# Kernel optimization log

Measured on AMD Instinct MI355X. Metric: run time of the kernel, lower is better.

The kernel has to match this reference:

```python
import jax, jax.numpy as jnp
import numpy as np

N_NODES = 100000
N_EDGES = 1600000
IN_CH, CH1, CH2 = 256, 256, 128


def gcn_conv(x, W, b, src, dst, ew, n):
    """PyG GCNConv: h = x @ W; out[i] = sum_j norm_ij * h[j] + b, with self-loops
    (weight 1.0) and symmetric normalization D^-1/2 A D^-1/2."""
    loop = jnp.arange(n)
    src_f = jnp.concatenate([src, loop])
    dst_f = jnp.concatenate([dst, loop])
    ew_f = jnp.concatenate([ew, jnp.ones((n,), dtype=x.dtype)])
    deg = jax.ops.segment_sum(ew_f, dst_f, num_segments=n)  # weighted in-degree incl self-loop
    dinv = jnp.where(deg > 0, jax.lax.rsqrt(deg), 0.0)
    norm = dinv[src_f] * ew_f * dinv[dst_f]                  # [E+N]
    h = x @ W                                                # [N, C_out]
    msg = h[src_f] * norm[:, None]                           # gather + scale, [E+N, C_out]
    out = jax.ops.segment_sum(msg, dst_f, num_segments=n)   # scatter-add to targets
    return out + b


def setup_inputs() -> dict:
    key = jax.random.key(0)
    ks = jax.random.split(key, 7)
    x = jax.random.normal(ks[0], (N_NODES, IN_CH), dtype=jnp.float32)
    edge_index = jax.random.randint(ks[1], (2, N_EDGES), 0, N_NODES, dtype=jnp.int64)
    edge_weight = jax.random.uniform(ks[2], (N_EDGES,), dtype=jnp.float32)
    # Glorot-style init for GCN weights, zero bias (PyG defaults)
    W1 = jax.random.normal(ks[3], (IN_CH, CH1), dtype=jnp.float32) * (1.0 / np.sqrt(IN_CH))
    b1 = jnp.zeros((CH1,), dtype=jnp.float32)
    W2 = jax.random.normal(ks[4], (CH1, CH2), dtype=jnp.float32) * (1.0 / np.sqrt(CH1))
    b2 = jnp.zeros((CH2,), dtype=jnp.float32)
    return {"x": x, "edge_index": edge_index, "edge_weight": edge_weight,
            "W1": W1, "b1": b1, "W2": W2, "b2": b2}


def reference(x, edge_index, edge_weight, W1, b1, W2, b2):
    src, dst = edge_index[0], edge_index[1]
    n = x.shape[0]
    x1 = gcn_conv(x, W1, b1, src, dst, edge_weight, n)
    x1 = jax.nn.gelu(x1, approximate=False)  # torch F.gelu default is exact erf
    # dropout is identity in eval mode (deterministic reference)
    x2 = gcn_conv(x1, W2, b2, src, dst, edge_weight, n)
    return x2
```

## Files before the change

### kernel.cpp

```cpp
#include <hip/hip_runtime.h>
#include <math.h>


#define CH1 256
#define CH2 128
#define MAXDEG 64

using bf16x8 = __attribute__((ext_vector_type(8))) short;
using f32x4  = __attribute__((ext_vector_type(4))) float;

__device__ __forceinline__ ushort f2bf(float f) {
    unsigned u = __float_as_uint(f);
    u = u + 0x7fffu + ((u >> 16) & 1u);
    return (ushort)(u >> 16);
}
__device__ __forceinline__ float bf_lo(unsigned u) {
    return __uint_as_float(u << 16);
}
__device__ __forceinline__ float bf_hi(unsigned u) {
    return __uint_as_float(u & 0xffff0000u);
}
__device__ __forceinline__ float dinv_from(unsigned long long a) {
    return rsqrtf(1.0f + (float)(a & 0xFFFFFFFFFFull) * (1.0f / 16777216.0f));
}

__global__ void zero_acc(unsigned long long* acc, int n) {
    int i = blockIdx.x * blockDim.x + threadIdx.x;
    if (i < n) acc[i] = 0ull;
}

__global__ __launch_bounds__(256) void fused_count_cvt_w(
    const int* __restrict__ ei, const float* __restrict__ ew,
    unsigned long long* __restrict__ acc, int* __restrict__ rank,
    int E, int EB,
    const float* __restrict__ x, ushort* __restrict__ xb, int n8, int CB,
    const float* __restrict__ W1, ushort* __restrict__ W1T, int w1n, int W1B,
    const float* __restrict__ W2, ushort* __restrict__ W2T, int w2n) {
    int bid = blockIdx.x;
    if (bid < EB) {
        int base = bid * 256 + threadIdx.x;
        int stride = EB * 256;
        int e[8]; int d[8]; float w[8];
#pragma unroll
        for (int k = 0; k < 8; ++k) e[k] = base + k * stride;
#pragma unroll
        for (int k = 0; k < 8; ++k)
            if (e[k] < E) { d[k] = ei[E + e[k]]; w[k] = ew[e[k]]; }
        unsigned long long old[8];
#pragma unroll
        for (int k = 0; k < 8; ++k)
            if (e[k] < E) {
                unsigned fx = (unsigned)__float2uint_rn(w[k] * 16777216.0f);
                old[k] = atomicAdd(&acc[d[k]],
                                   (1ull << 40) | (unsigned long long)fx);
            }
#pragma unroll
        for (int k = 0; k < 8; ++k)
            if (e[k] < E) rank[e[k]] = (int)(old[k] >> 40);
    } else if (bid < EB + CB) {
        int i = (bid - EB) * 256 + threadIdx.x;
        if (i < n8) {
            float4 a = reinterpret_cast<const float4*>(x)[i * 2];
            float4 b = reinterpret_cast<const float4*>(x)[i * 2 + 1];
            uint4 o;
            o.x = (unsigned)f2bf(a.x) | ((unsigned)f2bf(a.y) << 16);
            o.y = (unsigned)f2bf(a.z) | ((unsigned)f2bf(a.w) << 16);
            o.z = (unsigned)f2bf(b.x) | ((unsigned)f2bf(b.y) << 16);
            o.w = (unsigned)f2bf(b.z) | ((unsigned)f2bf(b.w) << 16);
            reinterpret_cast<uint4*>(xb)[i] = o;
        }
    } else if (bid < EB + CB + W1B) {
        int idx = (bid - EB - CB) * 256 + threadIdx.x;
        if (idx < w1n) {
            int k = idx / CH1, nn = idx % CH1;
            W1T[nn * CH1 + k] = f2bf(W1[idx]);
        }
    } else {
        int idx = (bid - EB - CB - W1B) * 256 + threadIdx.x;
        if (idx < w2n) {
            int k = idx / CH2, nn = idx % CH2;
            W2T[nn * CH1 + k] = f2bf(W2[idx]);
        }
    }
}

__device__ __forceinline__ void gemm_body(const ushort* __restrict__ A,
                                          const ushort* __restrict__ BT,
                                          ushort* __restrict__ C,
                                          int M, int N, int K, int bx, int by) {
    __shared__ __align__(16) ushort Als[128 * 32];
    __shared__ __align__(16) ushort Bls[128 * 32];

    const int t = threadIdx.x;
    const int w = t >> 6;
    const int lane = t & 63;
    const int wr = w >> 1, wc = w & 1;
    const int row0 = bx * 128;
    const int col0 = by * 128;

    f32x4 acc[4][4] = {};

    for (int k0 = 0; k0 < K; k0 += 32) {
#pragma unroll
        for (int i = 0; i < 2; ++i) {
            int c = (w * 2 + i) * 64 + lane;
            int row = c >> 2;
            int kg = c & 3;
            int arow = row0 + row; if (arow > M - 1) arow = M - 1;
            const ushort* gA = A + (size_t)arow * K + k0 + kg * 8;
            const ushort* gB = BT + (size_t)(col0 + row) * K + k0 + kg * 8;
            __builtin_amdgcn_global_load_lds(
                (const __attribute__((address_space(1))) unsigned*)gA,
                (__attribute__((address_space(3))) unsigned*)&Als[(size_t)(w * 2 + i) * 512],
                16, 0, 0);
            __builtin_amdgcn_global_load_lds(
                (const __attribute__((address_space(1))) unsigned*)gB,
                (__attribute__((address_space(3))) unsigned*)&Bls[(size_t)(w * 2 + i) * 512],
                16, 0, 0);
        }
        __syncthreads();

        bf16x8 afr[4], bfr[4];
#pragma unroll
        for (int m = 0; m < 4; ++m)
            afr[m] = *reinterpret_cast<const bf16x8*>(
                &Als[(wr * 64 + m * 16 + (lane & 15)) * 32 + (lane >> 4) * 8]);
#pragma unroll
        for (int nn = 0; nn < 4; ++nn)
            bfr[nn] = *reinterpret_cast<const bf16x8*>(
                &Bls[(wc * 64 + nn * 16 + (lane & 15)) * 32 + (lane >> 4) * 8]);
#pragma unroll
        for (int m = 0; m < 4; ++m)
#pragma unroll
            for (int nn = 0; nn < 4; ++nn)
                acc[m][nn] = __builtin_amdgcn_mfma_f32_16x16x32_bf16(
                    afr[m], bfr[nn], acc[m][nn], 0, 0, 0);
        __syncthreads();
    }

#pragma unroll
    for (int m = 0; m < 4; ++m) {
#pragma unroll
        for (int nn = 0; nn < 4; ++nn) {
            f32x4 v = acc[m][nn];
            int col = col0 + wc * 64 + nn * 16 + (lane & 15);
#pragma unroll
            for (int j = 0; j < 4; ++j) {
                int row = row0 + wr * 64 + m * 16 + (lane >> 4) * 4 + j;
                if (row < M) C[(size_t)row * N + col] = f2bf(v[j]);
            }
        }
    }
}

__global__ __launch_bounds__(256) void gemm_bf16(const ushort* __restrict__ A,
                                                 const ushort* __restrict__ BT,
                                                 ushort* __restrict__ C,
                                                 int M, int N, int K) {
    gemm_body(A, BT, C, M, N, K, blockIdx.x, blockIdx.y);
}

__global__ __launch_bounds__(256) void scatter_gemm1(
    const int* __restrict__ ei, const float* __restrict__ ew,
    const unsigned long long* __restrict__ acc,
    const int* __restrict__ rank,
    int2* __restrict__ pairs, int E, int SB,
    const ushort* __restrict__ xb, const ushort* __restrict__ W1T,
    ushort* __restrict__ h, int M, int gx) {
    int bid = blockIdx.x;
    if (bid < SB) {
        int e = bid * 256 + threadIdx.x;
        if (e < E) {
            int s = ei[e];
            int d = ei[E + e];
            int r = min(rank[e], MAXDEG - 1);
            float dv = dinv_from(acc[s]);
            int2 p;
            p.x = s;
            p.y = __float_as_int(ew[e] * dv);
            pairs[(size_t)d * MAXDEG + r] = p;
        }
    } else {
        int g = bid - SB;
        gemm_body(xb, W1T, h, M, CH1, CH1, g % gx, g / gx);
    }
}

__device__ __forceinline__ float gelu_exact(float x) {
    return 0.5f * x * (1.0f + erff(x * 0.70710678118654752f));
}

template <int C, int APPLY_GELU, int OUT_BF16>
__global__ __launch_bounds__(256) void aggregate4(
    const ushort* __restrict__ h, const unsigned long long* __restrict__ acc64,
    const int2* __restrict__ pairs, const float* __restrict__ bias,
    void* __restrict__ outv, int n) {
    constexpr int LPE = C / 8;
    constexpr int EPG = 64 / LPE;
    int wid = threadIdx.x >> 6;
    int lane = threadIdx.x & 63;
    int g = lane / LPE;
    int l = lane % LPE;
    int node = blockIdx.x * 4 + wid;
    if (node >= n) return;

    unsigned long long a = acc64[node];
    int deg = min((int)(a >> 40), MAXDEG);
    float di = dinv_from(a);

    const int2* pb = pairs + (size_t)node * MAXDEG;
    const ushort* hl = h + l * 8;

    float acc[8];
#pragma unroll
    for (int c = 0; c < 8; ++c) acc[c] = 0.f;

    for (int t = 0; t < deg; t += 4 * EPG) {
        int2 pk[4];
        float cf[4];
        uint4 gv[4];
#pragma unroll
        for (int k = 0; k < 4; ++k) {
            int idx = t + k * EPG + g;
            int cl = min(idx, deg - 1);
            pk[k] = pb[cl];
            cf[k] = (idx < deg) ? __int_as_float(pk[k].y) : 0.f;
        }
#pragma unroll
        for (int k = 0; k < 4; ++k)
            gv[k] = *reinterpret_cast<const uint4*>(hl + (size_t)pk[k].x * C);
#pragma unroll
        for (int k = 0; k < 4; ++k) {
            acc[0] += cf[k] * bf_lo(gv[k].x);
            acc[1] += cf[k] * bf_hi(gv[k].x);
            acc[2] += cf[k] * bf_lo(gv[k].y);
            acc[3] += cf[k] * bf_hi(gv[k].y);
            acc[4] += cf[k] * bf_lo(gv[k].z);
            acc[5] += cf[k] * bf_hi(gv[k].z);
            acc[6] += cf[k] * bf_lo(gv[k].w);
            acc[7] += cf[k] * bf_hi(gv[k].w);
        }
    }

#pragma unroll
    for (int off = LPE; off < 64; off <<= 1) {
#pragma unroll
        for (int c = 0; c < 8; ++c) acc[c] += __shfl_xor(acc[c], off);
    }

    float d2 = di * di;
    uint4 sv = *reinterpret_cast<const uint4*>(hl + (size_t)node * C);
    float self[8] = {bf_lo(sv.x), bf_hi(sv.x), bf_lo(sv.y), bf_hi(sv.y),
                     bf_lo(sv.z), bf_hi(sv.z), bf_lo(sv.w), bf_hi(sv.w)};
    float4 bv0 = *reinterpret_cast<const float4*>(bias + l * 8);
    float4 bv1 = *reinterpret_cast<const float4*>(bias + l * 8 + 4);
    float bb[8] = {bv0.x, bv0.y, bv0.z, bv0.w, bv1.x, bv1.y, bv1.z, bv1.w};

    float res[8];
#pragma unroll
    for (int c = 0; c < 8; ++c) {
        float v = di * acc[c] + d2 * self[c] + bb[c];
        res[c] = APPLY_GELU ? gelu_exact(v) : v;
    }

    if (g == 0) {
        if constexpr (OUT_BF16) {
            uint4 o;
            o.x = (unsigned)f2bf(res[0]) | ((unsigned)f2bf(res[1]) << 16);
            o.y = (unsigned)f2bf(res[2]) | ((unsigned)f2bf(res[3]) << 16);
            o.z = (unsigned)f2bf(res[4]) | ((unsigned)f2bf(res[5]) << 16);
            o.w = (unsigned)f2bf(res[6]) | ((unsigned)f2bf(res[7]) << 16);
            *reinterpret_cast<uint4*>((ushort*)outv + (size_t)node * C + l * 8) = o;
        } else {
            float* op = (float*)outv + (size_t)node * C + l * 8;
            float4 o0 = {res[0], res[1], res[2], res[3]};
            float4 o1 = {res[4], res[5], res[6], res[7]};
            *reinterpret_cast<float4*>(op) = o0;
            *reinterpret_cast<float4*>(op + 4) = o1;
        }
    }
}

extern "C" void kernel_launch(void* const* d_in, const int* in_sizes, int n_in,
                              void* d_out, int out_size, void* d_ws, size_t ws_size,
                              hipStream_t stream) {
    const float* x  = (const float*)d_in[0];
    const int*   ei = (const int*)d_in[1];
    const float* ew = (const float*)d_in[2];
    const float* W1 = (const float*)d_in[3];
    const float* b1 = (const float*)d_in[4];
    const float* W2 = (const float*)d_in[5];
    const float* b2 = (const float*)d_in[6];
    float* out = (float*)d_out;

    int n = in_sizes[0] / CH1;
    int E = in_sizes[1] / 2;

    char* ws = (char*)d_ws;
    size_t off = 0;
    auto alloc = [&](size_t bytes) -> void* {
        void* p = ws + off;
        off += (bytes + 255) & ~(size_t)255;
        return p;
    };
    unsigned long long* acc64 = (unsigned long long*)alloc((size_t)n * 8);
    int*    rank     = (int*)alloc((size_t)E * 4);
    int2*   pairs    = (int2*)alloc((size_t)n * MAXDEG * 8);
    ushort* xb       = (ushort*)alloc((size_t)n * CH1 * 2);
    ushort* h        = (ushort*)alloc((size_t)n * CH1 * 2);
    ushort* x1b      = (ushort*)alloc((size_t)n * CH1 * 2);
    ushort* W1T      = (ushort*)alloc((size_t)CH1 * CH1 * 2);
    ushort* W2T      = (ushort*)alloc((size_t)CH2 * CH1 * 2);

    int gn = (n + 255) / 256;

    int EB = (E + 2047) / 2048;
    int n8 = n * CH1 / 8;
    int CB = (n8 + 255) / 256;
    int w1n = CH1 * CH1, W1B = (w1n + 255) / 256;
    int w2n = CH1 * CH2, W2B = (w2n + 255) / 256;
    zero_acc<<<gn, 256, 0, stream>>>(acc64, n);
    fused_count_cvt_w<<<EB + CB + W1B + W2B, 256, 0, stream>>>(
        ei, ew, acc64, rank, E, EB, x, xb, n8, CB,
        W1, W1T, w1n, W1B, W2, W2T, w2n);

    int SB = (E + 255) / 256;
    int gx = (n + 127) / 128;
    int G1B = gx * (CH1 / 128);
    scatter_gemm1<<<SB + G1B, 256, 0, stream>>>(ei, ew, acc64, rank,
                                                pairs, E, SB,
                                                xb, W1T, h, n, gx);

    int ngb = (n + 3) / 4;

    aggregate4<CH1, 1, 1><<<ngb, 256, 0, stream>>>(h, acc64, pairs, b1, x1b, n);

    dim3 g2(gx, CH2 / 128);
    gemm_bf16<<<g2, 256, 0, stream>>>(x1b, W2T, h, n, CH2, CH1);
    aggregate4<CH2, 0, 0><<<ngb, 256, 0, stream>>>(h, acc64, pairs, b2, out, n);
}
```

Baseline: 382.3 us.

## Fold source-side normalization into GEMM epilogue and write pairs during counting

Moves the dinv[src] factor out of the per-edge weights: GEMM1 scales each output row by its own dinv, and layer-1 aggregation multiplies its result by dinv again so GEMM2's output is already source-scaled. Because the edge weight no longer needs the source degree, pairs are written directly in the atomic counting kernel, which removes the rank array and the separate scatter pass, leaving GEMM1 as its own launch. The aggregate self term is rewritten as di*(acc+self). Edges beyond MAXDEG are now dropped instead of clamped into the last slot, and the pairs writes now sit on the atomic critical path.

```diff
diff --git a/kernel.cpp b/kernel.cpp
--- a/kernel.cpp
+++ b/kernel.cpp
@@ -31,7 +31,7 @@
 
 __global__ __launch_bounds__(256) void fused_count_cvt_w(
     const int* __restrict__ ei, const float* __restrict__ ew,
-    unsigned long long* __restrict__ acc, int* __restrict__ rank,
+    unsigned long long* __restrict__ acc, int2* __restrict__ pairs,
     int E, int EB,
     const float* __restrict__ x, ushort* __restrict__ xb, int n8, int CB,
     const float* __restrict__ W1, ushort* __restrict__ W1T, int w1n, int W1B,
@@ -40,12 +40,16 @@
     if (bid < EB) {
         int base = bid * 256 + threadIdx.x;
         int stride = EB * 256;
-        int e[8]; int d[8]; float w[8];
+        int e[8]; int s[8]; int d[8]; float w[8];
 #pragma unroll
         for (int k = 0; k < 8; ++k) e[k] = base + k * stride;
 #pragma unroll
         for (int k = 0; k < 8; ++k)
-            if (e[k] < E) { d[k] = ei[E + e[k]]; w[k] = ew[e[k]]; }
+            if (e[k] < E) {
+                s[k] = ei[e[k]];
+                d[k] = ei[E + e[k]];
+                w[k] = ew[e[k]];
+            }
         unsigned long long old[8];
 #pragma unroll
         for (int k = 0; k < 8; ++k)
@@ -56,7 +60,15 @@
             }
 #pragma unroll
         for (int k = 0; k < 8; ++k)
-            if (e[k] < E) rank[e[k]] = (int)(old[k] >> 40);
+            if (e[k] < E) {
+                int r = (int)(old[k] >> 40);
+                if (r < MAXDEG) {
+                    int2 p;
+                    p.x = s[k];
+                    p.y = __float_as_int(w[k]);
+                    pairs[(size_t)d[k] * MAXDEG + r] = p;
+                }
+            }
     } else if (bid < EB + CB) {
         int i = (bid - EB) * 256 + threadIdx.x;
         if (i < n8) {
@@ -84,10 +96,11 @@
     }
 }
 
-__device__ __forceinline__ void gemm_body(const ushort* __restrict__ A,
-                                          const ushort* __restrict__ BT,
-                                          ushort* __restrict__ C,
-                                          int M, int N, int K, int bx, int by) {
+template <int SCALE>
+__global__ __launch_bounds__(256) void gemm_bf16(
+    const ushort* __restrict__ A, const ushort* __restrict__ BT,
+    ushort* __restrict__ C, const unsigned long long* __restrict__ acc64,
+    int M, int N, int K) {
     __shared__ __align__(16) ushort Als[128 * 32];
     __shared__ __align__(16) ushort Bls[128 * 32];
 
@@ -95,8 +108,8 @@
     const int w = t >> 6;
     const int lane = t & 63;
     const int wr = w >> 1, wc = w & 1;
-    const int row0 = bx * 128;
-    const int col0 = by * 128;
+    const int row0 = blockIdx.x * 128;
+    const int col0 = blockIdx.y * 128;
 
     f32x4 acc[4][4] = {};
 
@@ -141,48 +154,18 @@
 #pragma unroll
     for (int m = 0; m < 4; ++m) {
 #pragma unroll
-        for (int nn = 0; nn < 4; ++nn) {
-            f32x4 v = acc[m][nn];
-            int col = col0 + wc * 64 + nn * 16 + (lane & 15);
-#pragma unroll
-            for (int j = 0; j < 4; ++j) {
-                int row = row0 + wr * 64 + m * 16 + (lane >> 4) * 4 + j;
-                if (row < M) C[(size_t)row * N + col] = f2bf(v[j]);
+        for (int j = 0; j < 4; ++j) {
+            int row = row0 + wr * 64 + m * 16 + (lane >> 4) * 4 + j;
+            if (row < M) {
+                float sc = 1.0f;
+                if constexpr (SCALE) sc = dinv_from(acc64[row]);
+#pragma unroll
+                for (int nn = 0; nn < 4; ++nn) {
+                    int col = col0 + wc * 64 + nn * 16 + (lane & 15);
+                    C[(size_t)row * N + col] = f2bf(acc[m][nn][j] * sc);
+                }
             }
         }
-    }
-}
-
-__global__ __launch_bounds__(256) void gemm_bf16(const ushort* __restrict__ A,
-                                                 const ushort* __restrict__ BT,
-                                                 ushort* __restrict__ C,
-                                                 int M, int N, int K) {
-    gemm_body(A, BT, C, M, N, K, blockIdx.x, blockIdx.y);
-}
-
-__global__ __launch_bounds__(256) void scatter_gemm1(
-    const int* __restrict__ ei, const float* __restrict__ ew,
-    const unsigned long long* __restrict__ acc,
-    const int* __restrict__ rank,
-    int2* __restrict__ pairs, int E, int SB,
-    const ushort* __restrict__ xb, const ushort* __restrict__ W1T,
-    ushort* __restrict__ h, int M, int gx) {
-    int bid = blockIdx.x;
-    if (bid < SB) {
-        int e = bid * 256 + threadIdx.x;
-        if (e < E) {
-            int s = ei[e];
-            int d = ei[E + e];
-            int r = min(rank[e], MAXDEG - 1);
-            float dv = dinv_from(acc[s]);
-            int2 p;
-            p.x = s;
-            p.y = __float_as_int(ew[e] * dv);
-            pairs[(size_t)d * MAXDEG + r] = p;
-        }
-    } else {
-        int g = bid - SB;
-        gemm_body(xb, W1T, h, M, CH1, CH1, g % gx, g / gx);
     }
 }
 
@@ -190,8 +173,8 @@
     return 0.5f * x * (1.0f + erff(x * 0.70710678118654752f));
 }
 
-template <int C, int APPLY_GELU, int OUT_BF16>
-__global__ __launch_bounds__(256) void aggregate4(
+template <int C, int APPLY_GELU, int SCALE_OUT, int OUT_BF16>
+__global__ __launch_bounds__(256) void aggregate5(
     const ushort* __restrict__ h, const unsigned long long* __restrict__ acc64,
     const int2* __restrict__ pairs, const float* __restrict__ bias,
     void* __restrict__ outv, int n) {
@@ -248,7 +231,6 @@
         for (int c = 0; c < 8; ++c) acc[c] += __shfl_xor(acc[c], off);
     }
 
-    float d2 = di * di;
     uint4 sv = *reinterpret_cast<const uint4*>(hl + (size_t)node * C);
     float self[8] = {bf_lo(sv.x), bf_hi(sv.x), bf_lo(sv.y), bf_hi(sv.y),
                      bf_lo(sv.z), bf_hi(sv.z), bf_lo(sv.w), bf_hi(sv.w)};
@@ -259,8 +241,10 @@
     float res[8];
 #pragma unroll
     for (int c = 0; c < 8; ++c) {
-        float v = di * acc[c] + d2 * self[c] + bb[c];
-        res[c] = APPLY_GELU ? gelu_exact(v) : v;
+        float v = di * (acc[c] + self[c]) + bb[c];
+        if (APPLY_GELU) v = gelu_exact(v);
+        if (SCALE_OUT) v = v * di;
+        res[c] = v;
     }
 
     if (g == 0) {
@@ -304,7 +288,6 @@
         return p;
     };
     unsigned long long* acc64 = (unsigned long long*)alloc((size_t)n * 8);
-    int*    rank     = (int*)alloc((size_t)E * 4);
     int2*   pairs    = (int2*)alloc((size_t)n * MAXDEG * 8);
     ushort* xb       = (ushort*)alloc((size_t)n * CH1 * 2);
     ushort* h        = (ushort*)alloc((size_t)n * CH1 * 2);
@@ -321,21 +304,17 @@
     int w2n = CH1 * CH2, W2B = (w2n + 255) / 256;
     zero_acc<<<gn, 256, 0, stream>>>(acc64, n);
     fused_count_cvt_w<<<EB + CB + W1B + W2B, 256, 0, stream>>>(
-        ei, ew, acc64, rank, E, EB, x, xb, n8, CB,
+        ei, ew, acc64, pairs, E, EB, x, xb, n8, CB,
         W1, W1T, w1n, W1B, W2, W2T, w2n);
 
-    int SB = (E + 255) / 256;
     int gx = (n + 127) / 128;
-    int G1B = gx * (CH1 / 128);
-    scatter_gemm1<<<SB + G1B, 256, 0, stream>>>(ei, ew, acc64, rank,
-                                                pairs, E, SB,
-                                                xb, W1T, h, n, gx);
-
     int ngb = (n + 3) / 4;
 
-    aggregate4<CH1, 1, 1><<<ngb, 256, 0, stream>>>(h, acc64, pairs, b1, x1b, n);
+    dim3 g1(gx, CH1 / 128);
+    gemm_bf16<1><<<g1, 256, 0, stream>>>(xb, W1T, h, acc64, n, CH1, CH1);
+    aggregate5<CH1, 1, 1, 1><<<ngb, 256, 0, stream>>>(h, acc64, pairs, b1, x1b, n);
 
     dim3 g2(gx, CH2 / 128);
-    gemm_bf16<<<g2, 256, 0, stream>>>(x1b, W2T, h, n, CH2, CH1);
-    aggregate4<CH2, 0, 0><<<ngb, 256, 0, stream>>>(h, acc64, pairs, b2, out, n);
-}
+    gemm_bf16<0><<<g2, 256, 0, stream>>>(x1b, W2T, h, acc64, n, CH2, CH1);
+    aggregate5<CH2, 0, 0, 0><<<ngb, 256, 0, stream>>>(h, acc64, pairs, b2, out, n);
+}
```

Result: faster. 374.3 us (-2.1%).
